# Optimization experiments

Hardware: AMD Instinct MI355X
Metric: run time of the kernel (lower is better)

## Reference

```python
import jax, jax.numpy as jnp
import numpy as np

T, L, C = 128, 32, 4
B, D = 32, 512


def _compute_content_matrix(T, L, C):
    # Precomputed sparse weighting tensor: for each (window start i, window end j),
    # C clip-averaging rows over the frames covered by that window.
    Wc = np.zeros((L, L, C, T), dtype=np.float32)
    for i in range(L):
        for j in range(i, L):
            window_size = j - i + 1
            window_start, num_frames = i * (T // L), window_size * (T // L)
            clip_size = max(1, num_frames // C)
            for c in range(min(C, num_frames)):
                s = window_start + c * clip_size
                Wc[i, j, c, s:s + clip_size] = 1.0 / clip_size
    return Wc


def setup_inputs() -> dict:
    key = jax.random.key(0)
    k1, k2 = jax.random.split(key)
    f = jax.random.normal(k1, (B, T, D), dtype=jnp.float32)
    moment_mask = jax.random.uniform(k2, (B, L, L), dtype=jnp.float32)
    Wc = jnp.asarray(_compute_content_matrix(T, L, C))
    return {"f": f, "moment_mask": moment_mask, "Wc": Wc}


def reference(f, moment_mask, Wc):
    # fc: [B, L, L, C, D] -- clip features per (start,end) window, masked
    fc = jnp.einsum('lmct,btd->blmcd', Wc, f) * moment_mask[:, :, :, None, None]
    # fm: [B, L, L, D] -- mean over clips
    fm = jnp.mean(fc, axis=3)
    # fb: [B, L, D] -- boundary features = non-overlapping avg pool of size T//L
    b, t, d = f.shape
    l = Wc.shape[0]
    fb = f.reshape(b, l, t // l, d).mean(axis=2)
    return (fc, fm, fb)
```

## Files before the change

kernel.cpp:

```cpp
#include <hip/hip_runtime.h>

#define TT 128
#define LL 32
#define CC 4
#define BB 32
#define DD 512
#define D4 (DD / 4)

__device__ __forceinline__ float4 diff_scale(float4 a, float4 b, float s) {
    return make_float4((a.x - b.x) * s, (a.y - b.y) * s,
                       (a.z - b.z) * s, (a.w - b.w) * s);
}

__global__ __launch_bounds__(256) void prefix_kernel(const float* __restrict__ f,
                                                     float* __restrict__ P) {
    int idx = blockIdx.x * 256 + threadIdx.x;
    int b = idx >> 9;
    int d = idx & (DD - 1);
    const float* fp = f + (size_t)b * TT * DD + d;
    float* Pp = P + (size_t)b * (TT + 1) * DD + d;
    float acc = 0.f;
    Pp[0] = 0.f;
#pragma unroll 8
    for (int t = 0; t < TT; ++t) {
        acc += fp[(size_t)t * DD];
        Pp[(size_t)(t + 1) * DD] = acc;
    }
}

__global__ __launch_bounds__(128) void fcfm_kernel(const float4* __restrict__ P4,
                                                   const float* __restrict__ mask,
                                                   float4* __restrict__ fc4,
                                                   float4* __restrict__ fm4) {
    int blk = blockIdx.x;
    int j = blk & (LL - 1);
    int i = (blk >> 5) & (LL - 1);
    int b = blk >> 10;
    int tid = threadIdx.x;
    float4* fc_out = fc4 + (size_t)blk * CC * D4;
    float4* fm_out = fm4 + (size_t)blk * D4;

    if (j < i) {
        float4 z = make_float4(0.f, 0.f, 0.f, 0.f);
#pragma unroll
        for (int c = 0; c < CC; ++c) fc_out[c * D4 + tid] = z;
        fm_out[tid] = z;
        return;
    }

    int ws = j - i + 1;
    float sc = mask[blk] / (float)ws;
    float sm = 0.25f * sc;
    const float4* Pb = P4 + (size_t)b * (TT + 1) * D4 + tid;
    int s0 = 4 * i;

    float4 p0 = Pb[(size_t)(s0) * D4];
    float4 p1 = Pb[(size_t)(s0 + ws) * D4];
    float4 p2 = Pb[(size_t)(s0 + 2 * ws) * D4];
    float4 p3 = Pb[(size_t)(s0 + 3 * ws) * D4];
    float4 p4 = Pb[(size_t)(s0 + 4 * ws) * D4];

    fc_out[0 * D4 + tid] = diff_scale(p1, p0, sc);
    fc_out[1 * D4 + tid] = diff_scale(p2, p1, sc);
    fc_out[2 * D4 + tid] = diff_scale(p3, p2, sc);
    fc_out[3 * D4 + tid] = diff_scale(p4, p3, sc);
    fm_out[tid]          = diff_scale(p4, p0, sm);
}

__global__ __launch_bounds__(256) void fb_kernel(const float4* __restrict__ P4,
                                                 float4* __restrict__ fb4) {
    int idx = blockIdx.x * 256 + threadIdx.x;
    int d4 = idx & (D4 - 1);
    int l = (idx >> 7) & (LL - 1);
    int b = idx >> 12;
    const float4* Pb = P4 + (size_t)b * (TT + 1) * D4 + d4;
    float4 hi = Pb[(size_t)(4 * l + 4) * D4];
    float4 lo = Pb[(size_t)(4 * l) * D4];
    fb4[idx] = diff_scale(hi, lo, 0.25f);
}

__global__ __launch_bounds__(256) void fcfm_direct(const float* __restrict__ f,
                                                   const float* __restrict__ mask,
                                                   float* __restrict__ fc,
                                                   float* __restrict__ fm) {
    int blk = blockIdx.x;
    int j = blk & (LL - 1);
    int i = (blk >> 5) & (LL - 1);
    int b = blk >> 10;
    int tid = threadIdx.x;
    float* fc_out = fc + (size_t)blk * CC * DD;
    float* fm_out = fm + (size_t)blk * DD;

    if (j < i) {
        float4 z = make_float4(0.f, 0.f, 0.f, 0.f);
        float4* fc4 = (float4*)fc_out;
#pragma unroll
        for (int k = 0; k < 2; ++k) fc4[tid + k * 256] = z;
        float4* fm4 = (float4*)fm_out;
        if (tid < DD / 4) fm4[tid] = z;
        return;
    }

    int ws = j - i + 1;
    float m = mask[blk];
    float sc = m / (float)ws;
    const float* fbase = f + (size_t)b * TT * DD;

#pragma unroll
    for (int r = 0; r < 2; ++r) {
        int dd = tid + r * 256;
        float tot = 0.f;
#pragma unroll
        for (int c = 0; c < CC; ++c) {
            float s = 0.f;
            int t0 = 4 * i + c * ws;
            for (int t = 0; t < ws; ++t) s += fbase[(size_t)(t0 + t) * DD + dd];
            fc_out[c * DD + dd] = s * sc;
            tot += s;
        }
        fm_out[dd] = tot * sc * 0.25f;
    }
}

__global__ __launch_bounds__(256) void fb_direct(const float* __restrict__ f,
                                                 float* __restrict__ fb) {
    int idx = blockIdx.x * 256 + threadIdx.x;
    int d = idx & (DD - 1);
    int l = (idx >> 9) & (LL - 1);
    int b = idx >> 14;
    const float* fp = f + (size_t)b * TT * DD + d;
    int t0 = 4 * l;
    fb[idx] = (fp[(size_t)t0 * DD] + fp[(size_t)(t0 + 1) * DD] +
               fp[(size_t)(t0 + 2) * DD] + fp[(size_t)(t0 + 3) * DD]) * 0.25f;
}

extern "C" void kernel_launch(void* const* d_in, const int* in_sizes, int n_in,
                              void* d_out, int out_size, void* d_ws, size_t ws_size,
                              hipStream_t stream) {
    const float* f    = (const float*)d_in[0];
    const float* mask = (const float*)d_in[1];

    float* out = (float*)d_out;
    const size_t fc_elems = (size_t)BB * LL * LL * CC * DD;
    const size_t fm_elems = (size_t)BB * LL * LL * DD;
    float* fc = out;
    float* fm = out + fc_elems;
    float* fb = out + fc_elems + fm_elems;

    const size_t P_bytes = (size_t)BB * (TT + 1) * DD * sizeof(float);

    if (ws_size >= P_bytes) {
        float* P = (float*)d_ws;
        prefix_kernel<<<(BB * DD) / 256, 256, 0, stream>>>(f, P);
        fcfm_kernel<<<BB * LL * LL, 128, 0, stream>>>((const float4*)P, mask,
                                                      (float4*)fc, (float4*)fm);
        fb_kernel<<<(BB * LL * D4) / 256, 256, 0, stream>>>((const float4*)P,
                                                            (float4*)fb);
    } else {
        fcfm_direct<<<BB * LL * LL, 256, 0, stream>>>(f, mask, fc, fm);
        fb_direct<<<(BB * LL * DD) / 256, 256, 0, stream>>>(f, fb);
    }
}
```

Before: 358.7 us.

## Fuse fc/fm/fb into one row-per-block kernel and vectorise prefix scan

The prefix-sum kernel now processes float4 columns with 64-thread blocks. The separate fc/fm and fb kernels are merged into one kernel where each block handles a whole (b,i) row, looping over j. It writes zeros for j<i and reuses the p0 load across all j. Block indices are swizzled so that neighbouring blocks take different batches. This removes one launch and most of the redundant P reads. In exchange the grid shrinks from 32768 to 1024 blocks, and work is unbalanced across rows because larger i has fewer valid windows.

```diff
diff --git a/kernel.cpp b/kernel.cpp
--- a/kernel.cpp
+++ b/kernel.cpp
@@ -12,71 +12,70 @@
                        (a.z - b.z) * s, (a.w - b.w) * s);
 }
 
-__global__ __launch_bounds__(256) void prefix_kernel(const float* __restrict__ f,
-                                                     float* __restrict__ P) {
-    int idx = blockIdx.x * 256 + threadIdx.x;
-    int b = idx >> 9;
-    int d = idx & (DD - 1);
-    const float* fp = f + (size_t)b * TT * DD + d;
-    float* Pp = P + (size_t)b * (TT + 1) * DD + d;
-    float acc = 0.f;
-    Pp[0] = 0.f;
-#pragma unroll 8
+__global__ __launch_bounds__(64) void prefix_kernel(const float4* __restrict__ f4,
+                                                    float4* __restrict__ P4) {
+    int idx = blockIdx.x * 64 + threadIdx.x;
+    int b = idx >> 7;
+    int d4 = idx & (D4 - 1);
+    const float4* fp = f4 + (size_t)b * TT * D4 + d4;
+    float4* Pp = P4 + (size_t)b * (TT + 1) * D4 + d4;
+    float4 acc = make_float4(0.f, 0.f, 0.f, 0.f);
+    Pp[0] = acc;
+#pragma unroll 16
     for (int t = 0; t < TT; ++t) {
-        acc += fp[(size_t)t * DD];
-        Pp[(size_t)(t + 1) * DD] = acc;
+        float4 v = fp[(size_t)t * D4];
+        acc.x += v.x; acc.y += v.y; acc.z += v.z; acc.w += v.w;
+        Pp[(size_t)(t + 1) * D4] = acc;
     }
 }
 
-__global__ __launch_bounds__(128) void fcfm_kernel(const float4* __restrict__ P4,
-                                                   const float* __restrict__ mask,
-                                                   float4* __restrict__ fc4,
-                                                   float4* __restrict__ fm4) {
-    int blk = blockIdx.x;
-    int j = blk & (LL - 1);
-    int i = (blk >> 5) & (LL - 1);
-    int b = blk >> 10;
+__global__ __launch_bounds__(128) void fused_kernel(const float4* __restrict__ P4,
+                                                    const float* __restrict__ mask,
+                                                    float4* __restrict__ fc4,
+                                                    float4* __restrict__ fm4,
+                                                    float4* __restrict__ fb4) {
+    int h = blockIdx.x;
+    int logical = ((h & 7) << 7) | (h >> 3);
+    int b = logical >> 5;
+    int i = logical & (LL - 1);
     int tid = threadIdx.x;
-    float4* fc_out = fc4 + (size_t)blk * CC * D4;
-    float4* fm_out = fm4 + (size_t)blk * D4;
 
-    if (j < i) {
-        float4 z = make_float4(0.f, 0.f, 0.f, 0.f);
-#pragma unroll
-        for (int c = 0; c < CC; ++c) fc_out[c * D4 + tid] = z;
-        fm_out[tid] = z;
-        return;
+    const float4* Pb = P4 + (size_t)b * (TT + 1) * D4 + tid;
+    size_t base = ((size_t)b * LL + i) * LL;
+    float4* fcb = fc4 + base * CC * D4 + tid;
+    float4* fmb = fm4 + base * D4 + tid;
+    const float* mrow = mask + base;
+
+    float4 z = make_float4(0.f, 0.f, 0.f, 0.f);
+    for (int j = 0; j < i; ++j) {
+        float4* o = fcb + (size_t)j * CC * D4;
+        o[0] = z; o[D4] = z; o[2 * D4] = z; o[3 * D4] = z;
+        fmb[(size_t)j * D4] = z;
     }
 
-    int ws = j - i + 1;
-    float sc = mask[blk] / (float)ws;
-    float sm = 0.25f * sc;
-    const float4* Pb = P4 + (size_t)b * (TT + 1) * D4 + tid;
     int s0 = 4 * i;
+    float4 p0 = Pb[(size_t)s0 * D4];
 
-    float4 p0 = Pb[(size_t)(s0) * D4];
-    float4 p1 = Pb[(size_t)(s0 + ws) * D4];
-    float4 p2 = Pb[(size_t)(s0 + 2 * ws) * D4];
-    float4 p3 = Pb[(size_t)(s0 + 3 * ws) * D4];
-    float4 p4 = Pb[(size_t)(s0 + 4 * ws) * D4];
+    {
+        float4 q = Pb[(size_t)(s0 + 4) * D4];
+        fb4[((size_t)b * LL + i) * D4 + tid] = diff_scale(q, p0, 0.25f);
+    }
 
-    fc_out[0 * D4 + tid] = diff_scale(p1, p0, sc);
-    fc_out[1 * D4 + tid] = diff_scale(p2, p1, sc);
-    fc_out[2 * D4 + tid] = diff_scale(p3, p2, sc);
-    fc_out[3 * D4 + tid] = diff_scale(p4, p3, sc);
-    fm_out[tid]          = diff_scale(p4, p0, sm);
-}
-
-__global__ __launch_bounds__(256) void fb_kernel(const float4* __restrict__ P4,
-                                                 float4* __restrict__ fb4) {
-    int idx = blockIdx.x * 256 + threadIdx.x;
-    int d4 = idx & (D4 - 1);
-    int l = (idx >> 7) & (LL - 1);
-    int b = idx >> 12;
-    const float4* Pb = P4 + (size_t)b * (TT + 1) * D4 + d4;
-    float4 hi = Pb[(size_t)(4 * l + 4) * D4];
-    float4 lo = Pb[(size_t)(4 * l) * D4];
-    fb4[idx] = diff_scale(hi, lo, 0.25f);
+    for (int j = i; j < LL; ++j) {
+        int ws = j - i + 1;
+        float4 p1 = Pb[(size_t)(s0 + ws) * D4];
+        float4 p2 = Pb[(size_t)(s0 + 2 * ws) * D4];
+        float4 p3 = Pb[(size_t)(s0 + 3 * ws) * D4];
+        float4 p4 = Pb[(size_t)(s0 + 4 * ws) * D4];
+        float sc = mrow[j] / (float)ws;
+        float sm = 0.25f * sc;
+        float4* o = fcb + (size_t)j * CC * D4;
+        o[0]      = diff_scale(p1, p0, sc);
+        o[D4]     = diff_scale(p2, p1, sc);
+        o[2 * D4] = diff_scale(p3, p2, sc);
+        o[3 * D4] = diff_scale(p4, p3, sc);
+        fmb[(size_t)j * D4] = diff_scale(p4, p0, sm);
+    }
 }
 
 __global__ __launch_bounds__(256) void fcfm_direct(const float* __restrict__ f,
@@ -93,17 +92,16 @@
 
     if (j < i) {
         float4 z = make_float4(0.f, 0.f, 0.f, 0.f);
-        float4* fc4 = (float4*)fc_out;
+        float4* fcv = (float4*)fc_out;
 #pragma unroll
-        for (int k = 0; k < 2; ++k) fc4[tid + k * 256] = z;
-        float4* fm4 = (float4*)fm_out;
-        if (tid < DD / 4) fm4[tid] = z;
+        for (int k = 0; k < 2; ++k) fcv[tid + k * 256] = z;
+        float4* fmv = (float4*)fm_out;
+        if (tid < DD / 4) fmv[tid] = z;
         return;
     }
 
     int ws = j - i + 1;
-    float m = mask[blk];
-    float sc = m / (float)ws;
+    float sc = mask[blk] / (float)ws;
     const float* fbase = f + (size_t)b * TT * DD;
 
 #pragma unroll
@@ -151,11 +149,11 @@
 
     if (ws_size >= P_bytes) {
         float* P = (float*)d_ws;
-        prefix_kernel<<<(BB * DD) / 256, 256, 0, stream>>>(f, P);
-        fcfm_kernel<<<BB * LL * LL, 128, 0, stream>>>((const float4*)P, mask,
-                                                      (float4*)fc, (float4*)fm);
-        fb_kernel<<<(BB * LL * D4) / 256, 256, 0, stream>>>((const float4*)P,
-                                                            (float4*)fb);
+        prefix_kernel<<<(BB * D4) / 64, 64, 0, stream>>>((const float4*)f,
+                                                         (float4*)P);
+        fused_kernel<<<BB * LL, 128, 0, stream>>>((const float4*)P, mask,
+                                                  (float4*)fc, (float4*)fm,
+                                                  (float4*)fb);
     } else {
         fcfm_direct<<<BB * LL * LL, 256, 0, stream>>>(f, mask, fc, fm);
         fb_direct<<<(BB * LL * DD) / 256, 256, 0, stream>>>(f, fb);
```

Result: slower. 409.1 us (+14.1%).
